# Kernel tuning notes

Hardware: AMD Instinct MI355X
Metric: run time of the kernel (lower is better)

Reference implementation:

```python
import jax, jax.numpy as jnp
import numpy as np

N, E = 50000, 300000
IN_DIM, CODE_DIM = 1024, 768
HID, HEADS, DH = 256, 4, 64
NUM_REL = 5
CODE_WEIGHT = 1.0


def setup_inputs() -> dict:
    key = jax.random.key(0)
    ks = jax.random.split(key, 24)
    p = lambda k, shape: jax.random.normal(k, shape, dtype=jnp.float32) * 0.05
    return {
        "x": jax.random.normal(ks[0], (N, IN_DIM), dtype=jnp.float32),
        "edge_index": jax.random.randint(ks[1], (2, E), 0, N, dtype=jnp.int64),
        "edge_type": jax.random.randint(ks[2], (E,), 0, NUM_REL, dtype=jnp.int64),
        "edge_weight": jax.random.uniform(ks[3], (E,), dtype=jnp.float32),
        "rel_emb": p(ks[4], (NUM_REL, HID)),
        "W_in": p(ks[5], (HID, IN_DIM)),
        "b_in": jnp.zeros((HID,), jnp.float32),
        "W1": p(ks[6], (HEADS * DH, HID)),
        "a1_src": p(ks[7], (HEADS, DH)),
        "a1_dst": p(ks[8], (HEADS, DH)),
        "b1": jnp.zeros((HEADS * DH,), jnp.float32),
        "W2": p(ks[9], (HEADS * DH, HID)),
        "a2_src": p(ks[10], (HEADS, DH)),
        "a2_dst": p(ks[11], (HEADS, DH)),
        "b2": jnp.zeros((HEADS * DH,), jnp.float32),
        "ln1_g": jnp.ones((HID,), jnp.float32),
        "ln1_b": jnp.zeros((HID,), jnp.float32),
        "ln2_g": jnp.ones((HID,), jnp.float32),
        "ln2_b": jnp.zeros((HID,), jnp.float32),
        "W_out": p(ks[12], (1, HID)),
        "b_out": jnp.zeros((1,), jnp.float32),
    }


def _layer_norm(x, g, b, eps=1e-5):
    m = x.mean(-1, keepdims=True)
    v = ((x - m) ** 2).mean(-1, keepdims=True)
    return (x - m) * jax.lax.rsqrt(v + eps) * g + b


def _gat_conv(h, s_all, d_all, W, a_src, a_dst, bias):
    # PyG GATConv (concat=True, negative_slope=0.2), self-loops already in s_all/d_all
    xh = (h @ W.T).reshape(N, HEADS, DH)                      # [N,H,DH]
    al_s = (xh * a_src).sum(-1)                                # [N,H]
    al_d = (xh * a_dst).sum(-1)                                # [N,H]
    e = jax.nn.leaky_relu(al_s[s_all] + al_d[d_all], 0.2)      # [E+N,H]
    mx = jax.ops.segment_max(e, d_all, num_segments=N)         # segment softmax over dst
    ex = jnp.exp(e - mx[d_all])
    den = jax.ops.segment_sum(ex, d_all, num_segments=N)
    alpha = ex / (den[d_all] + 1e-16)
    out = jax.ops.segment_sum(xh[s_all] * alpha[:, :, None], d_all, num_segments=N)
    return out.reshape(N, HEADS * DH) + bias


def reference(x, edge_index, edge_type, edge_weight, rel_emb, W_in, b_in,
              W1, a1_src, a1_dst, b1, W2, a2_src, a2_dst, b2,
              ln1_g, ln1_b, ln2_g, ln2_b, W_out, b_out):
    # split (code_at_front=True), standardize numeric, l2-normalize code
    x_code = x[:, :CODE_DIM]
    x_num = x[:, CODE_DIM:]
    m = x_num.mean(0, keepdims=True)
    s = jnp.maximum(x_num.std(0, ddof=1, keepdims=True), 1e-6)
    x_num = (x_num - m) / s
    nrm = jnp.maximum(jnp.linalg.norm(x_code, axis=1, keepdims=True), 1e-12)
    x_code = x_code / nrm
    xin = jnp.concatenate([x_num, CODE_WEIGHT * x_code], axis=-1)

    h = jax.nn.relu(xin @ W_in.T + b_in)                       # [N,HID]

    src, dst = edge_index[0], edge_index[1]
    rel = rel_emb[edge_type] * edge_weight[:, None]            # [E,HID]
    msg = h[src] + rel
    h = h.at[dst].add(msg)                                     # index_add

    loop = jnp.arange(N, dtype=src.dtype)                      # GATConv add_self_loops
    s_all = jnp.concatenate([src, loop])
    d_all = jnp.concatenate([dst, loop])

    h1 = _gat_conv(h, s_all, d_all, W1, a1_src, a1_dst, b1)
    h = _layer_norm(h1 + h, ln1_g, ln1_b)
    h2 = _gat_conv(h, s_all, d_all, W2, a2_src, a2_dst, b2)
    h = _layer_norm(h2 + h, ln2_g, ln2_b)
    return (h @ W_out.T + b_out).squeeze(-1)                   # [N]
```

## Files before the change

kernel.cpp:

```cpp
#include <hip/hip_runtime.h>
#include <math.h>

constexpr int NN   = 50000;
constexpr int EE   = 300000;
constexpr int IND  = 1024;
constexpr int CODE = 768;
constexpr int HID  = 256;

typedef __bf16 bf16_t;
typedef bf16_t bf16x8 __attribute__((ext_vector_type(8)));
typedef float  f32x4  __attribute__((ext_vector_type(4)));

__device__ __forceinline__ f32x4 mfma16(bf16x8 a, bf16x8 b, f32x4 c) {
    return __builtin_amdgcn_mfma_f32_16x16x32_bf16(a, b, c, 0, 0, 0);
}

#define GLOAD_LDS16(gp, lp) __builtin_amdgcn_global_load_lds(                         \
    (__attribute__((address_space(1))) void*)(gp),                                    \
    (__attribute__((address_space(3))) void*)(lp), 16, 0, 0)

__device__ __forceinline__ void cvt_split(f32x4 u0, f32x4 u1, bf16x8& hi, bf16x8& lo) {
    #pragma unroll
    for (int i = 0; i < 4; i++) {
        bf16_t h0 = (bf16_t)u0[i];
        hi[i]     = h0;
        lo[i]     = (bf16_t)(u0[i] - (float)h0);
        bf16_t h1 = (bf16_t)u1[i];
        hi[4 + i] = h1;
        lo[4 + i] = (bf16_t)(u1[i] - (float)h1);
    }
}

__global__ void colstats_kernel(const float* __restrict__ x, float* __restrict__ sums) {
    int col = threadIdx.x;
    float s = 0.f, s2 = 0.f;
    for (int row = blockIdx.x; row < NN; row += gridDim.x) {
        float v = x[(size_t)row * IND + CODE + col];
        s += v; s2 += v * v;
    }
    atomicAdd(&sums[col], s);
    atomicAdd(&sums[256 + col], s2);
}

__global__ void finalize_stats_kernel(const float* __restrict__ sums, float* __restrict__ mi) {
    int c = threadIdx.x;
    float mean = sums[c] / (float)NN;
    float var  = (sums[256 + c] - (float)NN * mean * mean) / (float)(NN - 1);
    float sd   = sqrtf(fmaxf(var, 0.f));
    sd = fmaxf(sd, 1e-6f);
    mi[c]       = mean;
    mi[256 + c] = 1.f / sd;
}

__global__ void rownorm_kernel(const float* __restrict__ x, float* __restrict__ invnorm) {
    int lane = threadIdx.x & 63;
    int wid  = threadIdx.x >> 6;
    int row  = blockIdx.x * 4 + wid;
    if (row >= NN) return;
    const float4* x4 = (const float4*)(x + (size_t)row * IND);
    float s = 0.f;
    #pragma unroll
    for (int i = 0; i < 3; i++) {
        float4 v = x4[lane + i * 64];
        s += v.x * v.x + v.y * v.y + v.z * v.z + v.w * v.w;
    }
    #pragma unroll
    for (int off = 32; off; off >>= 1) s += __shfl_xor(s, off);
    if (lane == 0) invnorm[row] = 1.f / fmaxf(sqrtf(s), 1e-12f);
}

__global__ void prep_w_kernel(const float* __restrict__ W, const float* __restrict__ stats,
                              const float* __restrict__ b_in, bf16_t* __restrict__ Wh,
                              bf16_t* __restrict__ Wl, float* __restrict__ cb)
{
    int c = blockIdx.x, t = threadIdx.x;
    const float* wr = W + (size_t)c * IND;
    bf16_t* wh = Wh + (size_t)c * IND;
    bf16_t* wl = Wl + (size_t)c * IND;
    for (int k = t; k < 768; k += 256) {
        float v = wr[256 + k];
        bf16_t h = (bf16_t)v;
        wh[k] = h; wl[k] = (bf16_t)(v - (float)h);
    }
    {
        float v = wr[t] * stats[256 + t];
        bf16_t h = (bf16_t)v;
        wh[768 + t] = h; wl[768 + t] = (bf16_t)(v - (float)h);
    }
    float p = wr[t] * stats[256 + t] * stats[t];
    #pragma unroll
    for (int off = 32; off; off >>= 1) p += __shfl_xor(p, off);
    __shared__ float ps[4];
    if ((t & 63) == 0) ps[t >> 6] = p;
    __syncthreads();
    if (t == 0) cb[c] = b_in[c] - (ps[0] + ps[1] + ps[2] + ps[3]);
}

__global__ void prep_ws_kernel(const float* __restrict__ W, bf16_t* __restrict__ Wh,
                               bf16_t* __restrict__ Wl)
{
    int c = blockIdx.x, t = threadIdx.x;
    float v = W[(size_t)c * 256 + t];
    bf16_t h = (bf16_t)v;
    Wh[(size_t)c * 256 + t] = h;
    Wl[(size_t)c * 256 + t] = (bf16_t)(v - (float)h);
}


__device__ __forceinline__ void stage_a(const float* __restrict__ src, int ldk,
                                        int rowbase, int maxrow, int k0,
                                        float* ldsbuf, int tid) {
    int w = tid >> 6, l = tid & 63;
    int lr = l >> 3, lc = l & 7;
    int g  = lc ^ lr;
    #pragma unroll
    for (int i = 0; i < 4; i++) {
        int rloc = i * 32 + w * 8;
        float* dst = ldsbuf + rloc * 32;
        int row = rowbase + rloc + lr;
        if (row > maxrow) row = maxrow;
        const float* gp = src + (size_t)row * ldk + k0 + g * 4;
        GLOAD_LDS16(gp, dst);
    }
}

__device__ __forceinline__ void stage_b(const bf16_t* __restrict__ src, int n0, int ldk,
                                        int k0, bf16_t* buf, int tid) {
    int w = tid >> 6, l = tid & 63;
    #pragma unroll
    for (int i = 0; i < 2; i++) {
        int gbase = w * 128 + i * 64;
        bf16_t* dst = buf + gbase * 8;
        int g = gbase + l;
        int col = g >> 2, p = g & 3;
        int gs = p ^ ((col >> 1) & 3);
        const bf16_t* gp = src + (size_t)(n0 + col) * ldk + k0 + gs * 8;
        GLOAD_LDS16(gp, dst);
    }
}

template<int MODE, int K, int FATTN>
__global__ __launch_bounds__(256) void gemm_mfma_kernel(
    const float* __restrict__ A, const bf16_t* __restrict__ Bh,
    const bf16_t* __restrict__ Bl, const float* __restrict__ cb,
    const float* __restrict__ invnorm, const float* __restrict__ a_src,
    const float* __restrict__ a_dst, float* __restrict__ out,
    bf16_t* __restrict__ xhb, float* __restrict__ al_s, float* __restrict__ al_d)
{
    __shared__ float  As[2][128 * 32];
    __shared__ bf16_t Bhs[2][128 * 32];
    __shared__ bf16_t Bls[2][128 * 32];
    __shared__ float inv_s[128];
    constexpr int NT = K / 32;

    int tid  = threadIdx.x;
    int lane = tid & 63;
    int w    = tid >> 6;
    int wr   = w >> 1, wc = w & 1;
    int r0   = blockIdx.x * 128, n0 = blockIdx.y * 128;

    if (MODE == 1 && tid < 128) {
        int r = r0 + tid;
        inv_s[tid] = (r < NN) ? invnorm[r] : 1.f;
    }

    f32x4 acc[4][4];
    #pragma unroll
    for (int i = 0; i < 4; i++)
        #pragma unroll
        for (int j = 0; j < 4; j++) acc[i][j] = (f32x4)0.f;

    int kc = lane >> 4, fr = lane & 15;

    stage_a(A, K, r0, NN - 1, 0, As[0], tid);
    stage_b(Bh, n0, K, 0, Bhs[0], tid);
    stage_b(Bl, n0, K, 0, Bls[0], tid);
    __syncthreads();

    for (int t = 0; t < NT; ++t) {
        int buf = t & 1;
        if (t + 1 < NT) {
            stage_a(A, K, r0, NN - 1, (t + 1) * 32, As[buf ^ 1], tid);
            stage_b(Bh, n0, K, (t + 1) * 32, Bhs[buf ^ 1], tid);
            stage_b(Bl, n0, K, (t + 1) * 32, Bls[buf ^ 1], tid);
        }
        if (MODE == 1 && t == 24) {
            #pragma unroll
            for (int mf = 0; mf < 4; mf++) {
                f32x4 iv = *(const f32x4*)&inv_s[wr * 64 + mf * 16 + kc * 4];
                #pragma unroll
                for (int nf = 0; nf < 4; nf++)
                    #pragma unroll
                    for (int j = 0; j < 4; j++) acc[mf][nf][j] *= iv[j];
            }
        }
        const float*  Ab = As[buf];
        const bf16_t* Hb = Bhs[buf];
        const bf16_t* Lb = Bls[buf];
        bf16x8 ahi[4], alo[4];
        #pragma unroll
        for (int mf = 0; mf < 4; mf++) {
            int r  = wr * 64 + mf * 16 + fr;
            int rb = r * 32, r7 = r & 7;
            f32x4 u0 = *(const f32x4*)&Ab[rb + (((2 * kc + 0) ^ r7) << 2)];
            f32x4 u1 = *(const f32x4*)&Ab[rb + (((2 * kc + 1) ^ r7) << 2)];
            cvt_split(u0, u1, ahi[mf], alo[mf]);
        }
        #pragma unroll
        for (int nf = 0; nf < 4; nf++) {
            int c  = wc * 64 + nf * 16 + fr;
            int pr = kc ^ ((c >> 1) & 3);
            bf16x8 bhi = *(const bf16x8*)&Hb[c * 32 + pr * 8];
            bf16x8 blo = *(const bf16x8*)&Lb[c * 32 + pr * 8];
            #pragma unroll
            for (int mf = 0; mf < 4; mf++) {
                acc[mf][nf] = mfma16(ahi[mf], bhi, acc[mf][nf]);
                acc[mf][nf] = mfma16(alo[mf], bhi, acc[mf][nf]);
                acc[mf][nf] = mfma16(ahi[mf], blo, acc[mf][nf]);
            }
        }
        __syncthreads();
    }

    int head = blockIdx.y * 2 + wc;
    float asv[4], adv[4];
    if (FATTN) {
        #pragma unroll
        for (int nf = 0; nf < 4; nf++) {
            asv[nf] = a_src[head * 64 + nf * 16 + fr];
            adv[nf] = a_dst[head * 64 + nf * 16 + fr];
        }
    }
    #pragma unroll
    for (int mf = 0; mf < 4; mf++) {
        #pragma unroll
        for (int j = 0; j < 4; j++) {
            int row = r0 + wr * 64 + mf * 16 + kc * 4 + j;
            bool ok = row < NN;
            float s = 0.f, d = 0.f;
            #pragma unroll
            for (int nf = 0; nf < 4; nf++) {
                int col = n0 + wc * 64 + nf * 16 + fr;
                float v = acc[mf][nf][j];
                if (MODE == 1) {
                    v = fmaxf(v + cb[col], 0.f);
                    if (ok) out[(size_t)row * HID + col] = v;
                }
                if (FATTN) {
                    s += v * asv[nf]; d += v * adv[nf];
                    if (ok) xhb[(size_t)row * HID + col] = (bf16_t)v;
                }
            }
            if (FATTN) {
                #pragma unroll
                for (int off = 1; off < 16; off <<= 1) {
                    s += __shfl_xor(s, off);
                    d += __shfl_xor(d, off);
                }
                if (ok && fr == 0) {
                    al_s[row * 4 + head] = s;
                    al_d[row * 4 + head] = d;
                }
            }
        }
    }
}

__global__ void deg_kernel(const int* __restrict__ ei, int* __restrict__ deg) {
    int e = blockIdx.x * 256 + threadIdx.x;
    if (e < EE) atomicAdd(&deg[ei[EE + e]], 1);
}

constexpr int SCB = 1024;
constexpr int SCN = (NN + SCB - 1) / SCB;

__global__ void scan_pass1(const int* __restrict__ deg, int* __restrict__ bsum) {
    int b = blockIdx.x, t = threadIdx.x;
    int base = b * SCB + t * 4;
    int s = 0;
    #pragma unroll
    for (int i = 0; i < 4; i++) { int idx = base + i; if (idx < NN) s += deg[idx]; }
    #pragma unroll
    for (int off = 32; off; off >>= 1) s += __shfl_xor(s, off);
    __shared__ int ps[4];
    if ((t & 63) == 0) ps[t >> 6] = s;
    __syncthreads();
    if (t == 0) bsum[b] = ps[0] + ps[1] + ps[2] + ps[3];
}

__global__ void scan_pass2(int* __restrict__ bsum) {
    int t = threadIdx.x;
    int orig = (t < SCN) ? bsum[t] : 0;
    int v = orig;
    for (int off = 1; off < 64; off <<= 1) {
        int u = __shfl_up(v, off);
        if (t >= off) v += u;
    }
    if (t < SCN) bsum[t] = v - orig;
}

__global__ void scan_pass3(const int* __restrict__ deg, const int* __restrict__ boffs,
                           int* __restrict__ row_ptr, int* __restrict__ cursor) {
    int b = blockIdx.x, t = threadIdx.x;
    int base = b * SCB + t * 4;
    int d[4]; int tot = 0;
    #pragma unroll
    for (int i = 0; i < 4; i++) { int idx = base + i; d[i] = (idx < NN) ? deg[idx] : 0; tot += d[i]; }
    int v = tot;
    for (int off = 1; off < 64; off <<= 1) {
        int u = __shfl_up(v, off);
        if ((t & 63) >= off) v += u;
    }
    __shared__ int wsum[4];
    if ((t & 63) == 63) wsum[t >> 6] = v;
    __syncthreads();
    int woff = 0;
    for (int j = 0; j < (t >> 6); j++) woff += wsum[j];
    int run = boffs[b] + woff + v - tot;
    #pragma unroll
    for (int i = 0; i < 4; i++) {
        int idx = base + i;
        if (idx < NN) {
            cursor[idx] = run;
            run += d[i];
            row_ptr[idx + 1] = run;
        }
    }
    if (b == 0 && t == 0) row_ptr[0] = 0;
}

__global__ void fill_kernel(const int* __restrict__ ei, const int* __restrict__ etype,
                            const float* __restrict__ ew, int* __restrict__ cursor,
                            int* __restrict__ csr_src, int* __restrict__ csr_t,
                            float* __restrict__ csr_w) {
    int e = blockIdx.x * 256 + threadIdx.x;
    if (e >= EE) return;
    int dst = ei[EE + e];
    int pos = atomicAdd(&cursor[dst], 1);
    csr_src[pos] = ei[e];
    csr_t[pos]   = etype[e];
    csr_w[pos]   = ew[e];
}

__global__ void relagg_kernel(const float* __restrict__ h, const int* __restrict__ row_ptr,
                              const int* __restrict__ csr_src, const int* __restrict__ csr_t,
                              const float* __restrict__ csr_w,
                              const float* __restrict__ rel_emb, float* __restrict__ out)
{
    int lane = threadIdx.x & 63, wid = threadIdx.x >> 6;
    int node = blockIdx.x * 4 + wid;
    if (node >= NN) return;
    const float* hr = h + (size_t)node * HID;
    float acc[4];
    #pragma unroll
    for (int c = 0; c < 4; c++) acc[c] = hr[c * 64 + lane];
    float wsum[5] = {0.f, 0.f, 0.f, 0.f, 0.f};
    int beg = row_ptr[node], end = row_ptr[node + 1];
    int k = beg;
    for (; k + 4 <= end; k += 4) {
        int s[4], tt[4]; float ww[4];
        #pragma unroll
        for (int j = 0; j < 4; j++) {
            s[j]  = csr_src[k + j];
            tt[j] = csr_t[k + j];
            ww[j] = csr_w[k + j];
        }
        float xv[4][4];
        #pragma unroll
        for (int j = 0; j < 4; j++) {
            const float* hs = h + (size_t)s[j] * HID;
            #pragma unroll
            for (int c = 0; c < 4; c++) xv[j][c] = hs[c * 64 + lane];
        }
        #pragma unroll
        for (int j = 0; j < 4; j++) {
            #pragma unroll
            for (int c = 0; c < 4; c++) acc[c] += xv[j][c];
            #pragma unroll
            for (int r = 0; r < 5; r++) wsum[r] += (tt[j] == r) ? ww[j] : 0.f;
        }
    }
    for (; k < end; k++) {
        int src = csr_src[k]; int t = csr_t[k]; float w = csr_w[k];
        const float* hs = h + (size_t)src * HID;
        #pragma unroll
        for (int c = 0; c < 4; c++) acc[c] += hs[c * 64 + lane];
        #pragma unroll
        for (int r = 0; r < 5; r++) wsum[r] += (t == r) ? w : 0.f;
    }
    #pragma unroll
    for (int r = 0; r < 5; r++)
        #pragma unroll
        for (int c = 0; c < 4; c++) acc[c] += wsum[r] * rel_emb[r * HID + c * 64 + lane];
    float* o = out + (size_t)node * HID;
    #pragma unroll
    for (int c = 0; c < 4; c++) o[c * 64 + lane] = acc[c];
}

template<int FINAL>
__global__ void gat_kernel(const bf16_t* __restrict__ xhb, const float* __restrict__ al_s,
                           const float* __restrict__ al_d, const int* __restrict__ row_ptr,
                           const int* __restrict__ csr_src, const float* __restrict__ h_res,
                           const float* __restrict__ bias, const float* __restrict__ ln_g,
                           const float* __restrict__ ln_b, float* __restrict__ out,
                           const float* __restrict__ W_out, const float* __restrict__ b_out,
                           float* __restrict__ final_out)
{
    int lane = threadIdx.x & 63, wid = threadIdx.x >> 6;
    int node = blockIdx.x * 4 + wid;
    if (node >= NN) return;

    float4 aldv = *(const float4*)&al_d[node * 4];
    float ald[4] = {aldv.x, aldv.y, aldv.z, aldv.w};
    float m[4], den[4], acc[4];

    {
        float4 alsv = *(const float4*)&al_s[node * 4];
        float als[4] = {alsv.x, alsv.y, alsv.z, alsv.w};
        const bf16_t* xs = xhb + (size_t)node * HID;
        #pragma unroll
        for (int hh = 0; hh < 4; hh++) {
            float e = als[hh] + ald[hh];
            e = (e >= 0.f) ? e : 0.2f * e;
            m[hh] = e; den[hh] = 1.f;
            acc[hh] = (float)xs[hh * 64 + lane];
        }
    }

    int beg = row_ptr[node], end = row_ptr[node + 1];
    int k = beg;
    for (; k + 4 <= end; k += 4) {
        int s[4];
        #pragma unroll
        for (int j = 0; j < 4; j++) s[j] = csr_src[k + j];
        float4 av[4];
        #pragma unroll
        for (int j = 0; j < 4; j++) av[j] = *(const float4*)&al_s[s[j] * 4];
        float xv[4][4];
        #pragma unroll
        for (int j = 0; j < 4; j++) {
            const bf16_t* xs = xhb + (size_t)s[j] * HID;
            #pragma unroll
            for (int hh = 0; hh < 4; hh++) xv[j][hh] = (float)xs[hh * 64 + lane];
        }
        #pragma unroll
        for (int j = 0; j < 4; j++) {
            float als[4] = {av[j].x, av[j].y, av[j].z, av[j].w};
            #pragma unroll
            for (int hh = 0; hh < 4; hh++) {
                float e = als[hh] + ald[hh];
                e = (e >= 0.f) ? e : 0.2f * e;
                float mn  = fmaxf(m[hh], e);
                float f   = __expf(m[hh] - mn);
                float wgt = __expf(e - mn);
                m[hh]   = mn;
                den[hh] = den[hh] * f + wgt;
                acc[hh] = acc[hh] * f + wgt * xv[j][hh];
            }
        }
    }
    for (; k < end; k++) {
        int src = csr_src[k];
        float4 alsv = *(const float4*)&al_s[src * 4];
        float als[4] = {alsv.x, alsv.y, alsv.z, alsv.w};
        const bf16_t* xs = xhb + (size_t)src * HID;
        #pragma unroll
        for (int hh = 0; hh < 4; hh++) {
            float e = als[hh] + ald[hh];
            e = (e >= 0.f) ? e : 0.2f * e;
            float mn  = fmaxf(m[hh], e);
            float f   = __expf(m[hh] - mn);
            float wgt = __expf(e - mn);
            m[hh]   = mn;
            den[hh] = den[hh] * f + wgt;
            acc[hh] = acc[hh] * f + wgt * (float)xs[hh * 64 + lane];
        }
    }

    float z[4];
    #pragma unroll
    for (int hh = 0; hh < 4; hh++) {
        int c = hh * 64 + lane;
        z[hh] = acc[hh] / (den[hh] + 1e-16f) + bias[c] + h_res[(size_t)node * HID + c];
    }
    float s = z[0] + z[1] + z[2] + z[3];
    #pragma unroll
    for (int off = 32; off; off >>= 1) s += __shfl_xor(s, off);
    float mean = s * (1.f / 256.f);
    float vp = 0.f;
    #pragma unroll
    for (int hh = 0; hh < 4; hh++) { float d2 = z[hh] - mean; vp += d2 * d2; }
    #pragma unroll
    for (int off = 32; off; off >>= 1) vp += __shfl_xor(vp, off);
    float rstd = rsqrtf(vp * (1.f / 256.f) + 1e-5f);

    if (FINAL) {
        float dot = 0.f;
        #pragma unroll
        for (int hh = 0; hh < 4; hh++) {
            int c = hh * 64 + lane;
            float v = (z[hh] - mean) * rstd * ln_g[c] + ln_b[c];
            dot += v * W_out[c];
        }
        #pragma unroll
        for (int off = 32; off; off >>= 1) dot += __shfl_xor(dot, off);
        if (lane == 0) final_out[node] = dot + b_out[0];
    } else {
        #pragma unroll
        for (int hh = 0; hh < 4; hh++) {
            int c = hh * 64 + lane;
            out[(size_t)node * HID + c] = (z[hh] - mean) * rstd * ln_g[c] + ln_b[c];
        }
    }
}

extern "C" void kernel_launch(void* const* d_in, const int* in_sizes, int n_in,
                              void* d_out, int out_size, void* d_ws, size_t ws_size,
                              hipStream_t stream) {
    const float* x       = (const float*)d_in[0];
    const int*   ei      = (const int*)d_in[1];
    const int*   etype   = (const int*)d_in[2];
    const float* ew      = (const float*)d_in[3];
    const float* rel_emb = (const float*)d_in[4];
    const float* W_in    = (const float*)d_in[5];
    const float* b_in    = (const float*)d_in[6];
    const float* W1      = (const float*)d_in[7];
    const float* a1s     = (const float*)d_in[8];
    const float* a1d     = (const float*)d_in[9];
    const float* b1      = (const float*)d_in[10];
    const float* W2      = (const float*)d_in[11];
    const float* a2s     = (const float*)d_in[12];
    const float* a2d     = (const float*)d_in[13];
    const float* b2      = (const float*)d_in[14];
    const float* ln1g    = (const float*)d_in[15];
    const float* ln1b    = (const float*)d_in[16];
    const float* ln2g    = (const float*)d_in[17];
    const float* ln2b    = (const float*)d_in[18];
    const float* W_out   = (const float*)d_in[19];
    const float* b_out   = (const float*)d_in[20];
    float* out = (float*)d_out;

    char* ws = (char*)d_ws;
    auto alloc = [&](size_t bytes) {
        void* p = (void*)ws;
        ws += (bytes + 255) & ~(size_t)255;
        return p;
    };
    float*  bufA     = (float*)alloc((size_t)NN * HID * 4);
    float*  bufB     = (float*)alloc((size_t)NN * HID * 4);
    bf16_t* xhb      = (bf16_t*)alloc((size_t)NN * HID * 2);
    bf16_t* wmh      = (bf16_t*)alloc((size_t)HID * IND * 2);
    bf16_t* wml      = (bf16_t*)alloc((size_t)HID * IND * 2);
    bf16_t* w1h      = (bf16_t*)alloc((size_t)HID * HID * 2);
    bf16_t* w1l      = (bf16_t*)alloc((size_t)HID * HID * 2);
    bf16_t* w2h      = (bf16_t*)alloc((size_t)HID * HID * 2);
    bf16_t* w2l      = (bf16_t*)alloc((size_t)HID * HID * 2);
    float*  cbv      = (float*)alloc(256 * 4);
    float*  stats_s  = (float*)alloc(512 * 4);
    float*  stats_mi = (float*)alloc(512 * 4);
    float*  invnorm  = (float*)alloc((size_t)NN * 4);
    float*  al_s     = (float*)alloc((size_t)NN * 4 * 4);
    float*  al_d     = (float*)alloc((size_t)NN * 4 * 4);
    int*    deg      = (int*)alloc((size_t)NN * 4);
    int*    row_ptr  = (int*)alloc((size_t)(NN + 1) * 4);
    int*    cursor   = (int*)alloc((size_t)NN * 4);
    int*    csr_src  = (int*)alloc((size_t)EE * 4);
    int*    csr_t    = (int*)alloc((size_t)EE * 4);
    float*  csr_w    = (float*)alloc((size_t)EE * 4);
    int*    bsum     = (int*)alloc(64 * 4);

    hipMemsetAsync(stats_s, 0, 512 * 4, stream);
    hipMemsetAsync(deg, 0, (size_t)NN * 4, stream);

    colstats_kernel<<<1024, 256, 0, stream>>>(x, stats_s);
    finalize_stats_kernel<<<1, 256, 0, stream>>>(stats_s, stats_mi);
    rownorm_kernel<<<(NN + 3) / 4, 256, 0, stream>>>(x, invnorm);
    prep_w_kernel<<<256, 256, 0, stream>>>(W_in, stats_mi, b_in, wmh, wml, cbv);
    prep_ws_kernel<<<256, 256, 0, stream>>>(W1, w1h, w1l);
    prep_ws_kernel<<<256, 256, 0, stream>>>(W2, w2h, w2l);

    deg_kernel<<<(EE + 255) / 256, 256, 0, stream>>>(ei, deg);
    scan_pass1<<<SCN, 256, 0, stream>>>(deg, bsum);
    scan_pass2<<<1, 64, 0, stream>>>(bsum);
    scan_pass3<<<SCN, 256, 0, stream>>>(deg, bsum, row_ptr, cursor);
    fill_kernel<<<(EE + 255) / 256, 256, 0, stream>>>(ei, etype, ew, cursor,
                                                      csr_src, csr_t, csr_w);

    dim3 g1((NN + 127) / 128, 2);

    gemm_mfma_kernel<1, 1024, 0><<<g1, 256, 0, stream>>>(
        x, wmh, wml, cbv, invnorm, nullptr, nullptr, bufA, nullptr, nullptr, nullptr);

    int nodeBlocks = (NN + 3) / 4;

    relagg_kernel<<<nodeBlocks, 256, 0, stream>>>(bufA, row_ptr, csr_src, csr_t, csr_w,
                                                  rel_emb, bufB);

    gemm_mfma_kernel<0, 256, 1><<<g1, 256, 0, stream>>>(
        bufB, w1h, w1l, nullptr, nullptr, a1s, a1d, nullptr, xhb, al_s, al_d);
    gat_kernel<0><<<nodeBlocks, 256, 0, stream>>>(xhb, al_s, al_d, row_ptr, csr_src,
                                                  bufB, b1, ln1g, ln1b, bufA,
                                                  nullptr, nullptr, nullptr);

    gemm_mfma_kernel<0, 256, 1><<<g1, 256, 0, stream>>>(
        bufA, w2h, w2l, nullptr, nullptr, a2s, a2d, nullptr, xhb, al_s, al_d);
    gat_kernel<1><<<nodeBlocks, 256, 0, stream>>>(xhb, al_s, al_d, row_ptr, csr_src,
                                                  bufA, b2, ln2g, ln2b, nullptr,
                                                  W_out, b_out, out);
}
```

Measured before the change: 495.8 us.

## Drop low-bf16 weight term in input GEMM and vectorize gather kernels

For the MODE 1 GEMM, the B-low bf16 correction MFMA is removed along with its staging and shared buffer, leaving two MFMAs per fragment instead of three. This cuts MFMA work, LDS traffic and shared-memory use, at the cost of somewhat lower accuracy in that GEMM. The relation-aggregation and GAT aggregation kernels are rewritten so each lane owns four contiguous channels, using 16-byte (relagg) and 8-byte (GAT, 4 bf16) vector loads. In the GAT kernel each lane now handles a single head, so it keeps one softmax state instead of four.

```diff
diff --git a/kernel.cpp b/kernel.cpp
--- a/kernel.cpp
+++ b/kernel.cpp
@@ -8,6 +8,7 @@
 constexpr int HID  = 256;
 
 typedef __bf16 bf16_t;
+typedef bf16_t bf16x4 __attribute__((ext_vector_type(4)));
 typedef bf16_t bf16x8 __attribute__((ext_vector_type(8)));
 typedef float  f32x4  __attribute__((ext_vector_type(4)));
 
@@ -29,6 +30,13 @@
         hi[4 + i] = h1;
         lo[4 + i] = (bf16_t)(u1[i] - (float)h1);
     }
+}
+
+__device__ __forceinline__ f32x4 ld_bf4(const bf16_t* p) {
+    bf16x4 v = *(const bf16x4*)p;
+    f32x4 r;
+    r[0] = (float)v[0]; r[1] = (float)v[1]; r[2] = (float)v[2]; r[3] = (float)v[3];
+    return r;
 }
 
 __global__ void colstats_kernel(const float* __restrict__ x, float* __restrict__ sums) {
@@ -149,7 +157,8 @@
 {
     __shared__ float  As[2][128 * 32];
     __shared__ bf16_t Bhs[2][128 * 32];
-    __shared__ bf16_t Bls[2][128 * 32];
+    constexpr int BLN = (MODE == 1) ? 8 : 2 * 128 * 32;
+    __shared__ bf16_t Bls[BLN];
     __shared__ float inv_s[128];
     constexpr int NT = K / 32;
 
@@ -174,7 +183,7 @@
 
     stage_a(A, K, r0, NN - 1, 0, As[0], tid);
     stage_b(Bh, n0, K, 0, Bhs[0], tid);
-    stage_b(Bl, n0, K, 0, Bls[0], tid);
+    if (MODE == 0) stage_b(Bl, n0, K, 0, Bls, tid);
     __syncthreads();
 
     for (int t = 0; t < NT; ++t) {
@@ -182,7 +191,7 @@
         if (t + 1 < NT) {
             stage_a(A, K, r0, NN - 1, (t + 1) * 32, As[buf ^ 1], tid);
             stage_b(Bh, n0, K, (t + 1) * 32, Bhs[buf ^ 1], tid);
-            stage_b(Bl, n0, K, (t + 1) * 32, Bls[buf ^ 1], tid);
+            if (MODE == 0) stage_b(Bl, n0, K, (t + 1) * 32, Bls + (buf ^ 1) * (128 * 32), tid);
         }
         if (MODE == 1 && t == 24) {
             #pragma unroll
@@ -196,7 +205,7 @@
         }
         const float*  Ab = As[buf];
         const bf16_t* Hb = Bhs[buf];
-        const bf16_t* Lb = Bls[buf];
+        const bf16_t* Lb = Bls + buf * (128 * 32);
         bf16x8 ahi[4], alo[4];
         #pragma unroll
         for (int mf = 0; mf < 4; mf++) {
@@ -211,12 +220,16 @@
             int c  = wc * 64 + nf * 16 + fr;
             int pr = kc ^ ((c >> 1) & 3);
             bf16x8 bhi = *(const bf16x8*)&Hb[c * 32 + pr * 8];
-            bf16x8 blo = *(const bf16x8*)&Lb[c * 32 + pr * 8];
             #pragma unroll
             for (int mf = 0; mf < 4; mf++) {
                 acc[mf][nf] = mfma16(ahi[mf], bhi, acc[mf][nf]);
                 acc[mf][nf] = mfma16(alo[mf], bhi, acc[mf][nf]);
-                acc[mf][nf] = mfma16(ahi[mf], blo, acc[mf][nf]);
+            }
+            if (MODE == 0) {
+                bf16x8 blo = *(const bf16x8*)&Lb[c * 32 + pr * 8];
+                #pragma unroll
+                for (int mf = 0; mf < 4; mf++)
+                    acc[mf][nf] = mfma16(ahi[mf], blo, acc[mf][nf]);
             }
         }
         __syncthreads();
@@ -350,10 +363,8 @@
     int lane = threadIdx.x & 63, wid = threadIdx.x >> 6;
     int node = blockIdx.x * 4 + wid;
     if (node >= NN) return;
-    const float* hr = h + (size_t)node * HID;
-    float acc[4];
-    #pragma unroll
-    for (int c = 0; c < 4; c++) acc[c] = hr[c * 64 + lane];
+    int c0 = lane * 4;
+    f32x4 acc = *(const f32x4*)(h + (size_t)node * HID + c0);
     float wsum[5] = {0.f, 0.f, 0.f, 0.f, 0.f};
     int beg = row_ptr[node], end = row_ptr[node + 1];
     int k = beg;
@@ -365,36 +376,26 @@
             tt[j] = csr_t[k + j];
             ww[j] = csr_w[k + j];
         }
-        float xv[4][4];
+        f32x4 xv[4];
+        #pragma unroll
+        for (int j = 0; j < 4; j++) xv[j] = *(const f32x4*)(h + (size_t)s[j] * HID + c0);
         #pragma unroll
         for (int j = 0; j < 4; j++) {
-            const float* hs = h + (size_t)s[j] * HID;
-            #pragma unroll
-            for (int c = 0; c < 4; c++) xv[j][c] = hs[c * 64 + lane];
-        }
-        #pragma unroll
-        for (int j = 0; j < 4; j++) {
-            #pragma unroll
-            for (int c = 0; c < 4; c++) acc[c] += xv[j][c];
+            acc += xv[j];
             #pragma unroll
             for (int r = 0; r < 5; r++) wsum[r] += (tt[j] == r) ? ww[j] : 0.f;
         }
     }
     for (; k < end; k++) {
         int src = csr_src[k]; int t = csr_t[k]; float w = csr_w[k];
-        const float* hs = h + (size_t)src * HID;
-        #pragma unroll
-        for (int c = 0; c < 4; c++) acc[c] += hs[c * 64 + lane];
+        acc += *(const f32x4*)(h + (size_t)src * HID + c0);
         #pragma unroll
         for (int r = 0; r < 5; r++) wsum[r] += (t == r) ? w : 0.f;
     }
     #pragma unroll
     for (int r = 0; r < 5; r++)
-        #pragma unroll
-        for (int c = 0; c < 4; c++) acc[c] += wsum[r] * rel_emb[r * HID + c * 64 + lane];
-    float* o = out + (size_t)node * HID;
-    #pragma unroll
-    for (int c = 0; c < 4; c++) o[c * 64 + lane] = acc[c];
+        acc += wsum[r] * *(const f32x4*)(rel_emb + r * HID + c0);
+    *(f32x4*)(out + (size_t)node * HID + c0) = acc;
 }
 
 template<int FINAL>
@@ -409,22 +410,19 @@
     int lane = threadIdx.x & 63, wid = threadIdx.x >> 6;
     int node = blockIdx.x * 4 + wid;
     if (node >= NN) return;
-
-    float4 aldv = *(const float4*)&al_d[node * 4];
-    float ald[4] = {aldv.x, aldv.y, aldv.z, aldv.w};
-    float m[4], den[4], acc[4];
+    int hh = lane >> 4;
+    int c0 = lane * 4;
+
+    float ald = al_d[node * 4 + hh];
+    float m, den;
+    f32x4 acc;
 
     {
-        float4 alsv = *(const float4*)&al_s[node * 4];
-        float als[4] = {alsv.x, alsv.y, alsv.z, alsv.w};
-        const bf16_t* xs = xhb + (size_t)node * HID;
-        #pragma unroll
-        for (int hh = 0; hh < 4; hh++) {
-            float e = als[hh] + ald[hh];
-            e = (e >= 0.f) ? e : 0.2f * e;
-            m[hh] = e; den[hh] = 1.f;
-            acc[hh] = (float)xs[hh * 64 + lane];
-        }
+        float als = al_s[node * 4 + hh];
+        float e = als + ald;
+        e = (e >= 0.f) ? e : 0.2f * e;
+        m = e; den = 1.f;
+        acc = ld_bf4(xhb + (size_t)node * HID + c0);
     }
 
     int beg = row_ptr[node], end = row_ptr[node + 1];
@@ -433,84 +431,72 @@
         int s[4];
         #pragma unroll
         for (int j = 0; j < 4; j++) s[j] = csr_src[k + j];
-        float4 av[4];
-        #pragma unroll
-        for (int j = 0; j < 4; j++) av[j] = *(const float4*)&al_s[s[j] * 4];
-        float xv[4][4];
+        float als[4];
+        #pragma unroll
+        for (int j = 0; j < 4; j++) als[j] = al_s[s[j] * 4 + hh];
+        f32x4 xv[4];
+        #pragma unroll
+        for (int j = 0; j < 4; j++) xv[j] = ld_bf4(xhb + (size_t)s[j] * HID + c0);
         #pragma unroll
         for (int j = 0; j < 4; j++) {
-            const bf16_t* xs = xhb + (size_t)s[j] * HID;
-            #pragma unroll
-            for (int hh = 0; hh < 4; hh++) xv[j][hh] = (float)xs[hh * 64 + lane];
-        }
-        #pragma unroll
-        for (int j = 0; j < 4; j++) {
-            float als[4] = {av[j].x, av[j].y, av[j].z, av[j].w};
-            #pragma unroll
-            for (int hh = 0; hh < 4; hh++) {
-                float e = als[hh] + ald[hh];
-                e = (e >= 0.f) ? e : 0.2f * e;
-                float mn  = fmaxf(m[hh], e);
-                float f   = __expf(m[hh] - mn);
-                float wgt = __expf(e - mn);
-                m[hh]   = mn;
-                den[hh] = den[hh] * f + wgt;
-                acc[hh] = acc[hh] * f + wgt * xv[j][hh];
-            }
+            float e = als[j] + ald;
+            e = (e >= 0.f) ? e : 0.2f * e;
+            float mn  = fmaxf(m, e);
+            float f   = __expf(m - mn);
+            float wgt = __expf(e - mn);
+            m   = mn;
+            den = den * f + wgt;
+            acc = acc * f + wgt * xv[j];
         }
     }
     for (; k < end; k++) {
         int src = csr_src[k];
-        float4 alsv = *(const float4*)&al_s[src * 4];
-        float als[4] = {alsv.x, alsv.y, alsv.z, alsv.w};
-        const bf16_t* xs = xhb + (size_t)src * HID;
-        #pragma unroll
-        for (int hh = 0; hh < 4; hh++) {
-            float e = als[hh] + ald[hh];
-            e = (e >= 0.f) ? e : 0.2f * e;
-            float mn  = fmaxf(m[hh], e);
-            float f   = __expf(m[hh] - mn);
-            float wgt = __expf(e - mn);
-            m[hh]   = mn;
-            den[hh] = den[hh] * f + wgt;
-            acc[hh] = acc[hh] * f + wgt * (float)xs[hh * 64 + lane];
-        }
-    }
-
-    float z[4];
-    #pragma unroll
-    for (int hh = 0; hh < 4; hh++) {
-        int c = hh * 64 + lane;
-        z[hh] = acc[hh] / (den[hh] + 1e-16f) + bias[c] + h_res[(size_t)node * HID + c];
-    }
+        float als = al_s[src * 4 + hh];
+        f32x4 xv = ld_bf4(xhb + (size_t)src * HID + c0);
+        float e = als + ald;
+        e = (e >= 0.f) ? e : 0.2f * e;
+        float mn  = fmaxf(m, e);
+        float f   = __expf(m - mn);
+        float wgt = __expf(e - mn);
+        m   = mn;
+        den = den * f + wgt;
+        acc = acc * f + wgt * xv;
+    }
+
+    f32x4 bia = *(const f32x4*)(bias + c0);
+    f32x4 res = *(const f32x4*)(h_res + (size_t)node * HID + c0);
+    f32x4 z;
+    float rd = 1.f / (den + 1e-16f);
+    #pragma unroll
+    for (int i = 0; i < 4; i++) z[i] = acc[i] * rd + bia[i] + res[i];
+
     float s = z[0] + z[1] + z[2] + z[3];
     #pragma unroll
     for (int off = 32; off; off >>= 1) s += __shfl_xor(s, off);
     float mean = s * (1.f / 256.f);
     float vp = 0.f;
     #pragma unroll
-    for (int hh = 0; hh < 4; hh++) { float d2 = z[hh] - mean; vp += d2 * d2; }
+    for (int i = 0; i < 4; i++) { float d2 = z[i] - mean; vp += d2 * d2; }
     #pragma unroll
     for (int off = 32; off; off >>= 1) vp += __shfl_xor(vp, off);
     float rstd = rsqrtf(vp * (1.f / 256.f) + 1e-5f);
 
+    f32x4 g = *(const f32x4*)(ln_g + c0);
+    f32x4 bb = *(const f32x4*)(ln_b + c0);
     if (FINAL) {
+        f32x4 wo = *(const f32x4*)(W_out + c0);
         float dot = 0.f;
         #pragma unroll
-        for (int hh = 0; hh < 4; hh++) {
-            int c = hh * 64 + lane;
-            float v = (z[hh] - mean) * rstd * ln_g[c] + ln_b[c];
-            dot += v * W_out[c];
-        }
+        for (int i = 0; i < 4; i++)
+            dot += ((z[i] - mean) * rstd * g[i] + bb[i]) * wo[i];
         #pragma unroll
         for (int off = 32; off; off >>= 1) dot += __shfl_xor(dot, off);
         if (lane == 0) final_out[node] = dot + b_out[0];
     } else {
-        #pragma unroll
-        for (int hh = 0; hh < 4; hh++) {
-            int c = hh * 64 + lane;
-            out[(size_t)node * HID + c] = (z[hh] - mean) * rstd * ln_g[c] + ln_b[c];
-        }
+        f32x4 o;
+        #pragma unroll
+        for (int i = 0; i < 4; i++) o[i] = (z[i] - mean) * rstd * g[i] + bb[i];
+        *(f32x4*)(out + (size_t)node * HID + c0) = o;
     }
 }
 
```

New measurement: 445.3 us. 1.11x faster.
